# Performance work log

Measured on AMD Instinct MI355X. Metric: run time of the kernel, lower is better.

Reference implementation:

```python
import jax, jax.numpy as jnp
import numpy as np

B, T, D, H = 2, 2048, 1024, 16
HD = D // H


def sinusoidal_rel_pe(seq_len, d_model, dtype=jnp.float32):
    # Relative positions T-1 .. 0 (reversed), standard sin/cos interleave.
    pos = jnp.arange(seq_len - 1, -1, -1, dtype=jnp.float32)[:, None]  # [T,1]
    div = jnp.exp(-jnp.log(jnp.float32(10000.0)) * jnp.arange(0, d_model, 2, dtype=jnp.float32) / d_model)
    pe = jnp.zeros((seq_len, d_model), dtype=jnp.float32)
    pe = pe.at[:, 0::2].set(jnp.sin(pos * div))
    pe = pe.at[:, 1::2].set(jnp.cos(pos * div))
    return pe.astype(dtype)


def relative_to_absolute(x):
    # x: [B,H,T,L] with L == T. Music-Transformer skew trick.
    b, h, t1, l = x.shape
    x = jnp.pad(x, ((0, 0), (0, 0), (0, 0), (1, 0)))          # pad left of last dim
    x = x.reshape(b, h, -1)
    x = jnp.pad(x, ((0, 0), (0, 0), (l - t1, 0)))
    x = x.reshape(b, h, 1 + t1, l)
    return x[:, :, 1:]


def setup_inputs() -> dict:
    key = jax.random.key(0)
    k1, k2, k3 = jax.random.split(key, 3)
    x = jax.random.normal(k1, (B, T, D), dtype=jnp.float32)
    # causal mask: True where attention is disallowed (j > i)
    mask = jnp.triu(jnp.ones((T, T), dtype=bool), k=1)[None, None]
    mask = jnp.broadcast_to(mask, (B, 1, T, T))
    Wqkv = jax.random.normal(k2, (D, 3 * D), dtype=jnp.float32) * 0.02
    Wout = jax.random.normal(k3, (D, D), dtype=jnp.float32) * 0.02
    bout = jnp.zeros((D,), dtype=jnp.float32)
    return {"x": x, "mask": mask, "Wqkv": Wqkv, "Wout": Wout, "bout": bout}


def reference(x, mask, Wqkv, Wout, bout):
    b, t, d = x.shape
    scale = jnp.sqrt(jnp.float32(HD)).astype(x.dtype)
    qkv = x @ Wqkv                                  # [B,T,3D]
    q, k, v = jnp.split(qkv, 3, axis=-1)
    E = sinusoidal_rel_pe(t, d, x.dtype)            # [T,D], constant rel bias
    q = q.reshape(b, t, H, HD).transpose(0, 2, 1, 3)   # [B,H,T,hd]
    k = k.reshape(b, t, H, HD).transpose(0, 2, 1, 3)
    v = v.reshape(b, t, H, HD).transpose(0, 2, 1, 3)
    Eh = E.reshape(t, H, HD).transpose(1, 0, 2)        # [H,T,hd]
    att_k = jnp.einsum('bhqd,bhkd->bhqk', q, k)
    att_e = relative_to_absolute(jnp.einsum('bhqd,hkd->bhqk', q, Eh))
    score = (att_k + att_e) / scale
    score = jnp.where(mask, -jnp.inf, score)
    score = jax.nn.softmax(score, axis=-1)          # dropout is identity (eval)
    ctx = jnp.einsum('bhqk,bhkd->bhqd', score, v)
    ctx = ctx.transpose(0, 2, 1, 3).reshape(b, t, d)
    out = ctx @ Wout + bout
    return (out, score)
```

## Files before the change

kernel.cpp:

```cpp
#include <hip/hip_runtime.h>

typedef __bf16 bf16x8 __attribute__((ext_vector_type(8)));
typedef float f32x4 __attribute__((ext_vector_type(4)));

#define B_ 2
#define T_ 2048
#define D_ 1024
#define H_ 16

__device__ __forceinline__ ushort f2bf(float f) {
  union { float f; unsigned u; } v; v.f = f;
  unsigned u = v.u;
  return (ushort)((u + 0x7FFFu + ((u >> 16) & 1u)) >> 16);
}

__device__ __forceinline__ void g2l16(const void* g, void* l) {
  __builtin_amdgcn_global_load_lds(
      (const __attribute__((address_space(1))) unsigned int*)g,
      (__attribute__((address_space(3))) unsigned int*)l, 16, 0, 0);
}

__global__ __launch_bounds__(256) void cvt_kernel(const float* __restrict__ in,
                                                  ushort* __restrict__ out) {
  int i = (blockIdx.x * 256 + threadIdx.x) * 4;
  float4 v = *(const float4*)(in + i);
  ushort4 o;
  o.x = f2bf(v.x); o.y = f2bf(v.y); o.z = f2bf(v.z); o.w = f2bf(v.w);
  *(ushort4*)(out + i) = o;
}

__global__ void transpose_cvt(const float* __restrict__ in, ushort* __restrict__ out,
                              int R, int C) {
  __shared__ float tile[32][33];
  int bx = blockIdx.x * 32, by = blockIdx.y * 32;
  int tx = threadIdx.x, ty = threadIdx.y;
  for (int i = 0; i < 32; i += 8)
    tile[ty + i][tx] = in[(size_t)(by + ty + i) * C + (bx + tx)];
  __syncthreads();
  for (int i = 0; i < 32; i += 8)
    out[(size_t)(bx + ty + i) * R + (by + tx)] = f2bf(tile[tx][ty + i]);
}

__global__ __launch_bounds__(256) void gemm_bf16(
    const ushort* __restrict__ A, const ushort* __restrict__ BT,
    float* __restrict__ C, const float* __restrict__ bias,
    int M, int N, int K) {
  __shared__ alignas(16) ushort As[2][4096];
  __shared__ alignas(16) ushort Bs[2][4096];
  int tid = threadIdx.x;
  int wave = tid >> 6, lane = tid & 63;
  int l16 = lane & 15, lhi = lane >> 4;
  int m0 = blockIdx.y * 128, n0 = blockIdx.x * 128;
  int wr = (wave >> 1) * 64, wc = (wave & 1) * 64;
  int srow = lane >> 2, sch = lane & 3;

  f32x4 acc[4][4] = {};

  auto stage = [&](int kk, int buf) {
    for (int i = 0; i < 2; ++i) {
      int rg = i * 4 + wave;
      const ushort* ga = A + (size_t)(m0 + rg * 16 + srow) * K + kk + sch * 8;
      const ushort* gb = BT + (size_t)(n0 + rg * 16 + srow) * K + kk + sch * 8;
      g2l16(ga, &As[buf][rg * 512]);
      g2l16(gb, &Bs[buf][rg * 512]);
    }
  };

  stage(0, 0);
  int buf = 0;
  for (int kk = 0; kk < K; kk += 32) {
    __syncthreads();
    if (kk + 32 < K) stage(kk + 32, buf ^ 1);
    const ushort* Asb = As[buf];
    const ushort* Bsb = Bs[buf];
    bf16x8 af[4], bfr[4];
    for (int f = 0; f < 4; ++f)
      af[f] = *(const bf16x8*)(Asb + (wr + f * 16 + l16) * 32 + lhi * 8);
    for (int f = 0; f < 4; ++f)
      bfr[f] = *(const bf16x8*)(Bsb + (wc + f * 16 + l16) * 32 + lhi * 8);
    for (int fm = 0; fm < 4; ++fm)
      for (int fn = 0; fn < 4; ++fn)
        acc[fm][fn] = __builtin_amdgcn_mfma_f32_16x16x32_bf16(af[fm], bfr[fn], acc[fm][fn], 0, 0, 0);
    buf ^= 1;
  }
  for (int fm = 0; fm < 4; ++fm)
    for (int fn = 0; fn < 4; ++fn)
      for (int r = 0; r < 4; ++r) {
        int row = m0 + wr + fm * 16 + lhi * 4 + r;
        int col = n0 + wc + fn * 16 + l16;
        float v = acc[fm][fn][r];
        if (bias) v += bias[col];
        C[(size_t)row * N + col] = v;
      }
}

__global__ __launch_bounds__(256) void augment_kernel(
    const float* __restrict__ qkv,
    ushort* __restrict__ Qaug, ushort* __restrict__ Kaug, ushort* __restrict__ Vb) {
  int row = blockIdx.x;
  int b = row >> 11;
  int t = row & 2047;
  int tid = threadIdx.x;
  const float* src = qkv + (size_t)row * 3072;
  for (int i = 0; i < 4; ++i) {
    int idx = tid + i * 256;
    int h = idx >> 6, d = idx & 63;
    size_t obase = ((size_t)(b * H_ + h) * T_ + t);
    float q = src[idx];
    float k = src[1024 + idx];
    float v = src[2048 + idx];
    Qaug[obase * 128 + d] = f2bf(q * 0.125f);
    Kaug[obase * 128 + d] = f2bf(k);
    Vb[obase * 64 + d] = f2bf(v);
  }
  for (int i = 0; i < 2; ++i) {
    int idx = tid + i * 256;
    int h = idx >> 5, mm = idx & 31;
    int gdim = h * 64 + 2 * mm;
    float w = __expf(-9.2103403719761836f * (float)gdim * (1.0f / 1024.0f));
    float ang = w * (float)t;
    float si, co;
    __sincosf(ang, &si, &co);
    float qs = src[h * 64 + 2 * mm], qc = src[h * 64 + 2 * mm + 1];
    size_t obase = ((size_t)(b * H_ + h) * T_ + t);
    Qaug[obase * 128 + 64 + 2 * mm]     = f2bf((qs * si + qc * co) * 0.125f);
    Qaug[obase * 128 + 64 + 2 * mm + 1] = f2bf((qc * si - qs * co) * 0.125f);
    Kaug[obase * 128 + 64 + 2 * mm]     = f2bf(co);
    Kaug[obase * 128 + 64 + 2 * mm + 1] = f2bf(si);
  }
}

__global__ __launch_bounds__(256) void transpose_v(const ushort* __restrict__ Vb,
                                                   ushort* __restrict__ Vt) {
  __shared__ ushort tile[64][72];
  int bh = blockIdx.y, t0 = blockIdx.x * 64;
  int tid = threadIdx.x;
  for (int i = 0; i < 2; ++i) {
    int e = tid + i * 256;
    int row = e >> 3, ch = e & 7;
    *(int4*)(&tile[row][ch * 8]) =
        *(const int4*)(Vb + ((size_t)bh * T_ + t0 + row) * 64 + ch * 8);
  }
  __syncthreads();
  for (int i = 0; i < 2; ++i) {
    int e = tid + i * 256;
    int d = e >> 3, ch = e & 7;
    union { int4 v; ushort u[8]; } pk;
    for (int u = 0; u < 8; ++u) pk.u[u] = tile[ch * 8 + u][d];
    *(int4*)(Vt + ((size_t)bh * 64 + d) * T_ + t0 + ch * 8) = pk.v;
  }
}

__global__ __launch_bounds__(256) void attn_kernel(
    const ushort* __restrict__ Qaug,
    const ushort* __restrict__ Kaug,
    const ushort* __restrict__ Vt,
    float* __restrict__ score,
    ushort* __restrict__ ctxb) {
  int flat = blockIdx.y * 32 + blockIdx.x;
  int wg = (flat & 7) * 128 + (flat >> 3);
  int bh = wg >> 5;
  int qt = 31 - (wg & 31);
  int tid = threadIdx.x;
  int wave = tid >> 6, lane = tid & 63;
  int l16 = lane & 15, lhi = lane >> 4;
  int qb = wave * 16;
  int e7 = l16 & 7;

  __shared__ alignas(16) ushort Ks[2][8192];
  __shared__ alignas(16) ushort Vs[2][4096];
  __shared__ alignas(16) ushort Ps[2][4096];

  const ushort* Kbase = Kaug + (size_t)bh * T_ * 128;
  const ushort* Vbase = Vt + (size_t)bh * 64 * T_;

  auto stageK = [&](int kt, int buf) {
    for (int i = 0; i < 4; ++i) {
      int rg = i * 4 + wave;
      int key = rg * 4 + (lane >> 4);
      const ushort* g = Kbase + ((size_t)(kt * 64 + key)) * 128 + (((lane & 15) ^ (key & 7)) << 3);
      g2l16(g, &Ks[buf][rg * 512]);
    }
  };
  auto stageV = [&](int kt, int buf) {
    for (int i = 0; i < 2; ++i) {
      int rg = i * 4 + wave;
      int dim = rg * 8 + (lane >> 3);
      const ushort* g = Vbase + (size_t)dim * T_ + kt * 64 + (((lane & 7) ^ (dim & 7)) << 3);
      g2l16(g, &Vs[buf][rg * 512]);
    }
  };

  bf16x8 qf[4];
  {
    const ushort* Qg = Qaug + ((size_t)bh * T_ + qt * 64 + qb + l16) * 128;
    for (int ks = 0; ks < 4; ++ks)
      qf[ks] = *(const bf16x8*)(Qg + ks * 32 + lhi * 8);
  }

  stageK(0, 0);
  float plsum[4] = {0.f, 0.f, 0.f, 0.f};
  for (int kt = 0; kt <= qt; ++kt) {
    int buf = kt & 1;
    __syncthreads();
    if (kt < qt) stageK(kt + 1, buf ^ 1);
    const ushort* Kb = Ks[buf];
    f32x4 s[4] = {};
    for (int ks = 0; ks < 4; ++ks)
      for (int fn = 0; fn < 4; ++fn) {
        bf16x8 bfr = *(const bf16x8*)(Kb + (fn * 16 + l16) * 128 + ((((ks << 2) | lhi) ^ e7) << 3));
        s[fn] = __builtin_amdgcn_mfma_f32_16x16x32_bf16(qf[ks], bfr, s[fn], 0, 0, 0);
      }
    if (kt == qt) {
      for (int fn = 0; fn < 4; ++fn)
        for (int r = 0; r < 4; ++r)
          if (fn * 16 + l16 > qb + lhi * 4 + r) s[fn][r] = -1e30f;
    }
    for (int r = 0; r < 4; ++r)
      plsum[r] += __expf(s[0][r]) + __expf(s[1][r]) + __expf(s[2][r]) + __expf(s[3][r]);
  }
  float invl[4];
  for (int r = 0; r < 4; ++r) {
    float v = plsum[r];
    for (int dd = 1; dd < 16; dd <<= 1) v += __shfl_xor(v, dd);
    invl[r] = 1.f / v;
  }

  __syncthreads();
  stageK(0, 0);
  stageV(0, 0);
  f32x4 cacc[4] = {};
  float* srow = score + ((size_t)bh * T_ + (size_t)qt * 64) * T_;

  for (int kt = 0; kt <= qt; ++kt) {
    int buf = kt & 1;
    __syncthreads();
    if (kt < qt) { stageK(kt + 1, buf ^ 1); stageV(kt + 1, buf ^ 1); }
    const ushort* Kb = Ks[buf];
    f32x4 s[4] = {};
    for (int ks = 0; ks < 4; ++ks)
      for (int fn = 0; fn < 4; ++fn) {
        bf16x8 bfr = *(const bf16x8*)(Kb + (fn * 16 + l16) * 128 + ((((ks << 2) | lhi) ^ e7) << 3));
        s[fn] = __builtin_amdgcn_mfma_f32_16x16x32_bf16(qf[ks], bfr, s[fn], 0, 0, 0);
      }
    if (kt == qt) {
      for (int fn = 0; fn < 4; ++fn)
        for (int r = 0; r < 4; ++r)
          if (fn * 16 + l16 > qb + lhi * 4 + r) s[fn][r] = -1e30f;
    }
    ushort* Pb = Ps[buf];
    for (int fn = 0; fn < 4; ++fn)
      for (int r = 0; r < 4; ++r) {
        int row_loc = qb + lhi * 4 + r;
        float p = __expf(s[fn][r]) * invl[r];
        srow[(size_t)row_loc * T_ + kt * 64 + fn * 16 + l16] = p;
        Pb[row_loc * 64 + (((fn * 2 + (l16 >> 3)) ^ (row_loc & 7)) << 3) + e7] = f2bf(p);
      }
    asm volatile("s_waitcnt lgkmcnt(0)" ::: "memory");
    __builtin_amdgcn_sched_barrier(0);
    const ushort* Vb2 = Vs[buf];
    for (int ks = 0; ks < 2; ++ks) {
      bf16x8 pa = *(const bf16x8*)(Pb + (qb + l16) * 64 + ((((ks << 2) | lhi) ^ e7) << 3));
      for (int fn = 0; fn < 4; ++fn) {
        bf16x8 vb = *(const bf16x8*)(Vb2 + (fn * 16 + l16) * 64 + ((((ks << 2) | lhi) ^ e7) << 3));
        cacc[fn] = __builtin_amdgcn_mfma_f32_16x16x32_bf16(pa, vb, cacc[fn], 0, 0, 0);
      }
    }
  }

  {
    int row = tid >> 2, c16 = (tid & 3) * 16;
    float4 z = {0.f, 0.f, 0.f, 0.f};
    for (int kt = qt + 1; kt < 32; ++kt) {
      float* dst = srow + (size_t)row * T_ + kt * 64 + c16;
      for (int u = 0; u < 4; ++u) ((float4*)dst)[u] = z;
    }
  }

  int b = bh >> 4, h = bh & 15;
  for (int fn = 0; fn < 4; ++fn)
    for (int r = 0; r < 4; ++r) {
      int t = qt * 64 + qb + lhi * 4 + r;
      int col = h * 64 + fn * 16 + l16;
      ctxb[((size_t)(b * T_ + t)) * 1024 + col] = f2bf(cacc[fn][r]);
    }
}

extern "C" void kernel_launch(void* const* d_in, const int* in_sizes, int n_in,
                              void* d_out, int out_size, void* d_ws, size_t ws_size,
                              hipStream_t stream) {
  const float* x    = (const float*)d_in[0];
  const float* Wqkv = (const float*)d_in[2];
  const float* Wout = (const float*)d_in[3];
  const float* bout = (const float*)d_in[4];

  char* ws = (char*)d_ws;
  ushort* xb    = (ushort*)(ws + 0);
  ushort* wqkvT = (ushort*)(ws + 8388608);
  ushort* woutT = (ushort*)(ws + 14680064);
  float*  qkv   = (float*) (ws + 16777216);
  ushort* Qaug  = (ushort*)(ws + 67108864);
  ushort* Kaug  = (ushort*)(ws + 83886080);
  ushort* Vb    = (ushort*)(ws + 100663296);
  ushort* ctxb  = (ushort*)(ws + 109051904);
  ushort* Vt    = (ushort*)(ws + 16777216);

  float* out   = (float*)d_out;
  float* score = out + (size_t)4194304;

  cvt_kernel<<<4096, 256, 0, stream>>>(x, xb);
  dim3 tb(32, 8);
  transpose_cvt<<<dim3(3072 / 32, 1024 / 32), tb, 0, stream>>>(Wqkv, wqkvT, 1024, 3072);
  transpose_cvt<<<dim3(1024 / 32, 1024 / 32), tb, 0, stream>>>(Wout, woutT, 1024, 1024);
  gemm_bf16<<<dim3(24, 32), 256, 0, stream>>>(xb, wqkvT, qkv, nullptr, 4096, 3072, 1024);
  augment_kernel<<<4096, 256, 0, stream>>>(qkv, Qaug, Kaug, Vb);
  transpose_v<<<dim3(32, 32), 256, 0, stream>>>(Vb, Vt);
  attn_kernel<<<dim3(32, 32), 256, 0, stream>>>(Qaug, Kaug, Vt, score, ctxb);
  gemm_bf16<<<dim3(8, 32), 256, 0, stream>>>(ctxb, woutT, out, bout, 4096, 1024, 1024);
}
```

Baseline: 326.4 us.

## Drop V LDS staging, read V fragments from global, shrink shared memory

The attention kernel no longer copies V tiles into double-buffered LDS. Each wave now reads its V fragments straight from global memory. The P buffer is single-buffered, which is safe because each wave only touches its own rows, and launch bounds now request 4 blocks per SM. The goal is to cut LDS use and synchronization pressure so more workgroups can be resident and overlap the heavy score-matrix stores. The cost is that all four waves fetch the same V data through the cache hierarchy, and those loads are no longer prefetched ahead of the compute loop.

```diff
diff --git a/kernel.cpp b/kernel.cpp
--- a/kernel.cpp
+++ b/kernel.cpp
@@ -151,7 +151,7 @@
   }
 }
 
-__global__ __launch_bounds__(256) void attn_kernel(
+__global__ __launch_bounds__(256, 4) void attn_kernel(
     const ushort* __restrict__ Qaug,
     const ushort* __restrict__ Kaug,
     const ushort* __restrict__ Vt,
@@ -168,8 +168,7 @@
   int e7 = l16 & 7;
 
   __shared__ alignas(16) ushort Ks[2][8192];
-  __shared__ alignas(16) ushort Vs[2][4096];
-  __shared__ alignas(16) ushort Ps[2][4096];
+  __shared__ alignas(16) ushort Ps[4096];
 
   const ushort* Kbase = Kaug + (size_t)bh * T_ * 128;
   const ushort* Vbase = Vt + (size_t)bh * 64 * T_;
@@ -180,14 +179,6 @@
       int key = rg * 4 + (lane >> 4);
       const ushort* g = Kbase + ((size_t)(kt * 64 + key)) * 128 + (((lane & 15) ^ (key & 7)) << 3);
       g2l16(g, &Ks[buf][rg * 512]);
-    }
-  };
-  auto stageV = [&](int kt, int buf) {
-    for (int i = 0; i < 2; ++i) {
-      int rg = i * 4 + wave;
-      int dim = rg * 8 + (lane >> 3);
-      const ushort* g = Vbase + (size_t)dim * T_ + kt * 64 + (((lane & 7) ^ (dim & 7)) << 3);
-      g2l16(g, &Vs[buf][rg * 512]);
     }
   };
 
@@ -228,14 +219,13 @@
 
   __syncthreads();
   stageK(0, 0);
-  stageV(0, 0);
   f32x4 cacc[4] = {};
   float* srow = score + ((size_t)bh * T_ + (size_t)qt * 64) * T_;
 
   for (int kt = 0; kt <= qt; ++kt) {
     int buf = kt & 1;
     __syncthreads();
-    if (kt < qt) { stageK(kt + 1, buf ^ 1); stageV(kt + 1, buf ^ 1); }
+    if (kt < qt) stageK(kt + 1, buf ^ 1);
     const ushort* Kb = Ks[buf];
     f32x4 s[4] = {};
     for (int ks = 0; ks < 4; ++ks)
@@ -248,21 +238,19 @@
         for (int r = 0; r < 4; ++r)
           if (fn * 16 + l16 > qb + lhi * 4 + r) s[fn][r] = -1e30f;
     }
-    ushort* Pb = Ps[buf];
     for (int fn = 0; fn < 4; ++fn)
       for (int r = 0; r < 4; ++r) {
         int row_loc = qb + lhi * 4 + r;
         float p = __expf(s[fn][r]) * invl[r];
         srow[(size_t)row_loc * T_ + kt * 64 + fn * 16 + l16] = p;
-        Pb[row_loc * 64 + (((fn * 2 + (l16 >> 3)) ^ (row_loc & 7)) << 3) + e7] = f2bf(p);
+        Ps[row_loc * 64 + (((fn * 2 + (l16 >> 3)) ^ (row_loc & 7)) << 3) + e7] = f2bf(p);
       }
     asm volatile("s_waitcnt lgkmcnt(0)" ::: "memory");
     __builtin_amdgcn_sched_barrier(0);
-    const ushort* Vb2 = Vs[buf];
     for (int ks = 0; ks < 2; ++ks) {
-      bf16x8 pa = *(const bf16x8*)(Pb + (qb + l16) * 64 + ((((ks << 2) | lhi) ^ e7) << 3));
+      bf16x8 pa = *(const bf16x8*)(Ps + (qb + l16) * 64 + ((((ks << 2) | lhi) ^ e7) << 3));
       for (int fn = 0; fn < 4; ++fn) {
-        bf16x8 vb = *(const bf16x8*)(Vb2 + (fn * 16 + l16) * 64 + ((((ks << 2) | lhi) ^ e7) << 3));
+        bf16x8 vb = *(const bf16x8*)(Vbase + (size_t)(fn * 16 + l16) * T_ + kt * 64 + ks * 32 + lhi * 8);
         cacc[fn] = __builtin_amdgcn_mfma_f32_16x16x32_bf16(pa, vb, cacc[fn], 0, 0, 0);
       }
     }
@@ -270,10 +258,10 @@
 
   {
     int row = tid >> 2, c16 = (tid & 3) * 16;
-    float4 z = {0.f, 0.f, 0.f, 0.f};
+    f32x4 z = {0.f, 0.f, 0.f, 0.f};
     for (int kt = qt + 1; kt < 32; ++kt) {
-      float* dst = srow + (size_t)row * T_ + kt * 64 + c16;
-      for (int u = 0; u < 4; ++u) ((float4*)dst)[u] = z;
+      f32x4* dst = (f32x4*)(srow + (size_t)row * T_ + kt * 64 + c16);
+      for (int u = 0; u < 4; ++u) dst[u] = z;
     }
   }
 
```

After: 398.8 us. 22.2% more time.

## Replace __syncthreads with explicit vmcnt waits and barriers, single-buffer P tile

Applied to the files above, without the earlier changes.

Moves the per-iteration barrier to the end of each key tile and uses explicit s_waitcnt vmcnt plus s_barrier. In the second pass it waits with vmcnt(16), so the outstanding score stores need not drain before the next tile starts. The P staging buffer drops to a single LDS buffer, which reduces shared memory use. The risks are LDS race conditions: P is now reused across iterations, and the vmcnt counting must exactly match the number of outstanding global stores versus async LDS loads.

```diff
diff --git a/kernel.cpp b/kernel.cpp
--- a/kernel.cpp
+++ b/kernel.cpp
@@ -169,7 +169,7 @@
 
   __shared__ alignas(16) ushort Ks[2][8192];
   __shared__ alignas(16) ushort Vs[2][4096];
-  __shared__ alignas(16) ushort Ps[2][4096];
+  __shared__ alignas(16) ushort Ps[4096];
 
   const ushort* Kbase = Kaug + (size_t)bh * T_ * 128;
   const ushort* Vbase = Vt + (size_t)bh * 64 * T_;
@@ -199,11 +199,13 @@
   }
 
   stageK(0, 0);
+  asm volatile("s_waitcnt vmcnt(0)" ::: "memory");
+  __builtin_amdgcn_s_barrier();
   float plsum[4] = {0.f, 0.f, 0.f, 0.f};
   for (int kt = 0; kt <= qt; ++kt) {
     int buf = kt & 1;
-    __syncthreads();
     if (kt < qt) stageK(kt + 1, buf ^ 1);
+    __builtin_amdgcn_sched_barrier(0);
     const ushort* Kb = Ks[buf];
     f32x4 s[4] = {};
     for (int ks = 0; ks < 4; ++ks)
@@ -218,6 +220,10 @@
     }
     for (int r = 0; r < 4; ++r)
       plsum[r] += __expf(s[0][r]) + __expf(s[1][r]) + __expf(s[2][r]) + __expf(s[3][r]);
+    if (kt < qt) {
+      asm volatile("s_waitcnt vmcnt(0)" ::: "memory");
+      __builtin_amdgcn_s_barrier();
+    }
   }
   float invl[4];
   for (int r = 0; r < 4; ++r) {
@@ -226,16 +232,18 @@
     invl[r] = 1.f / v;
   }
 
-  __syncthreads();
+  __builtin_amdgcn_s_barrier();
   stageK(0, 0);
   stageV(0, 0);
+  asm volatile("s_waitcnt vmcnt(0)" ::: "memory");
+  __builtin_amdgcn_s_barrier();
   f32x4 cacc[4] = {};
   float* srow = score + ((size_t)bh * T_ + (size_t)qt * 64) * T_;
 
   for (int kt = 0; kt <= qt; ++kt) {
     int buf = kt & 1;
-    __syncthreads();
     if (kt < qt) { stageK(kt + 1, buf ^ 1); stageV(kt + 1, buf ^ 1); }
+    __builtin_amdgcn_sched_barrier(0);
     const ushort* Kb = Ks[buf];
     f32x4 s[4] = {};
     for (int ks = 0; ks < 4; ++ks)
@@ -248,32 +256,35 @@
         for (int r = 0; r < 4; ++r)
           if (fn * 16 + l16 > qb + lhi * 4 + r) s[fn][r] = -1e30f;
     }
-    ushort* Pb = Ps[buf];
     for (int fn = 0; fn < 4; ++fn)
       for (int r = 0; r < 4; ++r) {
         int row_loc = qb + lhi * 4 + r;
         float p = __expf(s[fn][r]) * invl[r];
         srow[(size_t)row_loc * T_ + kt * 64 + fn * 16 + l16] = p;
-        Pb[row_loc * 64 + (((fn * 2 + (l16 >> 3)) ^ (row_loc & 7)) << 3) + e7] = f2bf(p);
+        Ps[row_loc * 64 + (((fn * 2 + (l16 >> 3)) ^ (row_loc & 7)) << 3) + e7] = f2bf(p);
       }
     asm volatile("s_waitcnt lgkmcnt(0)" ::: "memory");
     __builtin_amdgcn_sched_barrier(0);
     const ushort* Vb2 = Vs[buf];
     for (int ks = 0; ks < 2; ++ks) {
-      bf16x8 pa = *(const bf16x8*)(Pb + (qb + l16) * 64 + ((((ks << 2) | lhi) ^ e7) << 3));
+      bf16x8 pa = *(const bf16x8*)(Ps + (qb + l16) * 64 + ((((ks << 2) | lhi) ^ e7) << 3));
       for (int fn = 0; fn < 4; ++fn) {
         bf16x8 vb = *(const bf16x8*)(Vb2 + (fn * 16 + l16) * 64 + ((((ks << 2) | lhi) ^ e7) << 3));
         cacc[fn] = __builtin_amdgcn_mfma_f32_16x16x32_bf16(pa, vb, cacc[fn], 0, 0, 0);
       }
     }
+    if (kt < qt) {
+      asm volatile("s_waitcnt vmcnt(16)" ::: "memory");
+      __builtin_amdgcn_s_barrier();
+    }
   }
 
   {
     int row = tid >> 2, c16 = (tid & 3) * 16;
-    float4 z = {0.f, 0.f, 0.f, 0.f};
+    f32x4 z = {0.f, 0.f, 0.f, 0.f};
     for (int kt = qt + 1; kt < 32; ++kt) {
-      float* dst = srow + (size_t)row * T_ + kt * 64 + c16;
-      for (int u = 0; u < 4; ++u) ((float4*)dst)[u] = z;
+      f32x4* dst = (f32x4*)(srow + (size_t)row * T_ + kt * 64 + c16);
+      for (int u = 0; u < 4; ++u) dst[u] = z;
     }
   }
 
```

Measured after the change: 316.3 us. -3.1%, faster.
